# Kernel optimization log

Measured on AMD Instinct MI355X. Metric: run time of the kernel, lower is better.

Reference implementation:

```python
import jax, jax.numpy as jnp
import numpy as np


def _closest_dist_sum(p1, p2):
    # p1: [B, N, 3], p2: [B, M, 3]
    # Euclidean distance via the expanded quadratic form; matches
    # torch.norm(p1 - p2, 2, dim=3) -> min over p2 -> sum over all.
    d2 = (jnp.sum(p1 * p1, axis=-1)[:, :, None]
          + jnp.sum(p2 * p2, axis=-1)[:, None, :]
          - 2.0 * jnp.einsum('bnd,bmd->bnm', p1, p2))  # [B, N, M]
    d = jnp.sqrt(jnp.maximum(d2, 0.0))
    return jnp.sum(jnp.min(d, axis=2))


def setup_inputs() -> dict:
    key = jax.random.key(0)
    k1, k2 = jax.random.split(key)
    shape_xyz = jax.random.normal(k1, (8, 8192, 6), dtype=jnp.float32)
    skel_xyz = jax.random.normal(k2, (8, 2048, 3), dtype=jnp.float32)
    return {"shape_xyz": shape_xyz, "skel_xyz": skel_xyz}


def reference(shape_xyz, skel_xyz):
    # normals (shape_xyz[:, :, 3:6]) are extracted but unused in the loss
    pts = shape_xyz[:, :, :3]
    cd1 = _closest_dist_sum(pts, skel_xyz)   # shape -> skeleton
    cd2 = _closest_dist_sum(skel_xyz, pts)   # skeleton -> shape
    loss_cd = (cd1 + cd2) * 0.0001
    return loss_cd
```

## Files before the change

kernel.cpp:

```cpp
#include <hip/hip_runtime.h>

#define BATCH   8
#define SHAPE_N 8192
#define SKEL_M  2048
#define CHUNK   1024

#define WS2_OFF 512

typedef short bf16x8 __attribute__((ext_vector_type(8)));
typedef float f32x16 __attribute__((ext_vector_type(16)));
union FragU { bf16x8 v; uint4 u4; };

__device__ __forceinline__ unsigned int f2bf(float a) {
    unsigned int u = __float_as_uint(a);
    return (u + 0x7FFFu + ((u >> 16) & 1u)) >> 16;
}
__device__ __forceinline__ float bf2f(unsigned int h) {
    return __uint_as_float(h << 16);
}
__device__ __forceinline__ unsigned int pack2(unsigned int lo, unsigned int hi) {
    return lo | (hi << 16);
}
__device__ __forceinline__ void bfsplit(float v, unsigned int& h, unsigned int& l) {
    h = f2bf(v);
    l = f2bf(v - bf2f(h));
}

template <int SA, int SB>
__device__ __forceinline__ float cd_scan(
    const float* __restrict__ Araw,
    const float* __restrict__ Braw,
    uint4* sB, float* p_ra)
{
    const int tid = threadIdx.x;
    const int l = tid & 63;

    const float* p = Araw + (size_t)(l & 31) * SA;
    const float x = p[0], y = p[1], z = p[2];
    *p_ra = x * x + y * y + z * z;
    unsigned int hx, lx, hy, ly, hz, lz;
    bfsplit(x, hx, lx); bfsplit(y, hy, ly); bfsplit(z, hz, lz);
    const unsigned int one = 0x3F80u;
    FragU bf;
    if (l < 32) {
        bf.u4 = make_uint4(pack2(hx, hy), pack2(hz, one),
                           pack2(lx, ly), pack2(lz, one));
    } else {
        bf.u4 = make_uint4(pack2(hx, hy), pack2(hz, 0u), 0u, 0u);
    }

    const f32x16 Z = {0,0,0,0,0,0,0,0,0,0,0,0,0,0,0,0};
    float rmin = 3.4e38f;
    const unsigned int off0 = (unsigned int)((l >> 5) * 512 + (l & 31) * 16);

    for (int c = 0; c < 2048; c += CHUNK) {
        __syncthreads();
        const float* src = Braw + (size_t)c * SB;
        for (int i = tid; i < CHUNK; i += 256) {
            const float* q = src + (size_t)i * SB;
            const float bx = q[0], by = q[1], bz = q[2];
            const float cx = -2.f * bx, cy = -2.f * by, cz = -2.f * bz;
            const float rb = bx * bx + by * by + bz * bz;
            unsigned int chx, clx, chy, cly, chz, clz, rbh, rbl;
            bfsplit(cx, chx, clx); bfsplit(cy, chy, cly); bfsplit(cz, chz, clz);
            bfsplit(rb, rbh, rbl);
            const int g = i >> 5, r = i & 31;
            sB[g * 64 + r]      = make_uint4(pack2(chx, chy), pack2(chz, rbh),
                                             pack2(chx, chy), pack2(chz, rbl));
            sB[g * 64 + 32 + r] = make_uint4(pack2(clx, cly), pack2(clz, 0u),
                                             0u, 0u);
        }
        __syncthreads();

        unsigned int o = off0;
#pragma unroll 8
        for (int g = 0; g < CHUNK / 32; ++g) {
            FragU af;
            af.u4 = *(const uint4*)((const char*)sB + o);
            o += 1024;
            f32x16 D = __builtin_amdgcn_mfma_f32_32x32x16_bf16(af.v, bf.v, Z, 0, 0, 0);
            const float t0 = fminf(fminf(D[0],  D[1]),  D[2]);
            const float t1 = fminf(fminf(D[3],  D[4]),  D[5]);
            const float t2 = fminf(fminf(D[6],  D[7]),  D[8]);
            const float t3 = fminf(fminf(D[9],  D[10]), D[11]);
            const float t4 = fminf(fminf(D[12], D[13]), D[14]);
            const float u0 = fminf(fminf(t0, t1), t2);
            const float u1 = fminf(fminf(t3, t4), D[15]);
            rmin = fminf(rmin, fminf(u0, u1));
        }
    }
    rmin = fminf(rmin, __shfl_xor(rmin, 32, 64));
    return rmin;
}

__global__ __launch_bounds__(256) void cd_main(
    const float* __restrict__ shape, const float* __restrict__ skel,
    float* __restrict__ ws)
{
    __shared__ uint4 sB[CHUNK * 2];
    __shared__ float s_wsum[4];
    const int tid = threadIdx.x;
    const int l = tid & 63, wv = tid >> 6;
    const int bid = blockIdx.x;

    if (bid < 512) {
        const int b = bid >> 6, sub = bid & 63;
        float ra;
        const float rmin = cd_scan<6, 3>(
            shape + ((size_t)b * SHAPE_N + sub * 128 + wv * 32) * 6,
            skel + (size_t)b * SKEL_M * 3, sB, &ra);
        float d = (l < 32) ? sqrtf(fmaxf(ra + rmin, 0.f)) : 0.f;
        for (int o = 32; o; o >>= 1) d += __shfl_down(d, o, 64);
        if (l == 0) s_wsum[wv] = d;
        __syncthreads();
        if (tid == 0)
            ws[bid] = s_wsum[0] + s_wsum[1] + s_wsum[2] + s_wsum[3];
    } else {
        const int j = bid - 512;
        const int b = j >> 6, rem = j & 63;
        const int asub = rem >> 2, bs = rem & 3;
        float ra;
        const float rmin = cd_scan<3, 6>(
            skel + ((size_t)b * SKEL_M + asub * 128 + wv * 32) * 3,
            shape + ((size_t)b * SHAPE_N + bs * 2048) * 6, sB, &ra);
        if (l < 32)
            ws[WS2_OFF + bs * (BATCH * SKEL_M) + b * SKEL_M +
               asub * 128 + wv * 32 + l] = ra + rmin;
    }
}

__global__ __launch_bounds__(1024) void cd_reduce(
    const float* __restrict__ ws, float* __restrict__ out)
{
    __shared__ float s_wsum[16];
    const int t = threadIdx.x;
    float s = 0.f;

    const float4* w4 = (const float4*)(ws + WS2_OFF);
#pragma unroll
    for (int r = 0; r < 4; ++r) {
        const int i4 = r * 1024 + t;
        float4 v0 = w4[i4];
        const float4 v1 = w4[4096 + i4];
        const float4 v2 = w4[8192 + i4];
        const float4 v3 = w4[12288 + i4];
        v0.x = fminf(fminf(v0.x, v1.x), fminf(v2.x, v3.x));
        v0.y = fminf(fminf(v0.y, v1.y), fminf(v2.y, v3.y));
        v0.z = fminf(fminf(v0.z, v1.z), fminf(v2.z, v3.z));
        v0.w = fminf(fminf(v0.w, v1.w), fminf(v2.w, v3.w));
        s += sqrtf(fmaxf(v0.x, 0.f)) + sqrtf(fmaxf(v0.y, 0.f)) +
             sqrtf(fmaxf(v0.z, 0.f)) + sqrtf(fmaxf(v0.w, 0.f));
    }
    if (t < 512) s += ws[t];

    for (int o = 32; o; o >>= 1) s += __shfl_down(s, o, 64);
    const int lane = t & 63, wave = t >> 6;
    if (lane == 0) s_wsum[wave] = s;
    __syncthreads();
    if (t == 0) {
        float tot = 0.f;
#pragma unroll
        for (int w = 0; w < 16; ++w) tot += s_wsum[w];
        out[0] = tot * 1e-4f;
    }
}

extern "C" void kernel_launch(void* const* d_in, const int* in_sizes, int n_in,
                              void* d_out, int out_size, void* d_ws, size_t ws_size,
                              hipStream_t stream) {
    const float* shape = (const float*)d_in[0];
    const float* skel  = (const float*)d_in[1];
    float* out         = (float*)d_out;
    float* ws          = (float*)d_ws;

    cd_main<<<1024, 256, 0, stream>>>(shape, skel, ws);
    cd_reduce<<<1, 1024, 0, stream>>>(ws, out);
}
```

Before: 75.07 us.

## Precompute bf16 point fragments and double-buffer async LDS loads with register-blocked MFMA

A new prep kernel converts every skeleton and shape point into split-bf16 MFMA fragments once and writes them to workspace, so the main kernel no longer redoes this conversion in each block. The main kernel then streams those fragments into LDS with global_load_lds into a double buffer, overlapping the next chunk's load with the current chunk's compute. Each wave now holds four A fragments and splits the B range by wave, so one LDS read feeds four MFMAs; per-wave minima are merged through shared memory. The cost is an extra kernel launch, workspace traffic for the precomputed fragments, and more registers per wave.

Result: faster. 73.60 us (-2.0%).

```diff
diff --git a/kernel.cpp b/kernel.cpp
--- a/kernel.cpp
+++ b/kernel.cpp
@@ -3,9 +3,11 @@
 #define BATCH   8
 #define SHAPE_N 8192
 #define SKEL_M  2048
-#define CHUNK   1024
+#define CHUNK   512
 
 #define WS2_OFF 512
+#define SKC_OFF 66048
+#define SHC_OFF (66048 + 131072)
 
 typedef short bf16x8 __attribute__((ext_vector_type(8)));
 typedef float f32x16 __attribute__((ext_vector_type(16)));
@@ -26,106 +28,179 @@
     l = f2bf(v - bf2f(h));
 }
 
-template <int SA, int SB>
-__device__ __forceinline__ float cd_scan(
-    const float* __restrict__ Araw,
-    const float* __restrict__ Braw,
-    uint4* sB, float* p_ra)
-{
-    const int tid = threadIdx.x;
-    const int l = tid & 63;
-
-    const float* p = Araw + (size_t)(l & 31) * SA;
-    const float x = p[0], y = p[1], z = p[2];
-    *p_ra = x * x + y * y + z * z;
-    unsigned int hx, lx, hy, ly, hz, lz;
-    bfsplit(x, hx, lx); bfsplit(y, hy, ly); bfsplit(z, hz, lz);
-    const unsigned int one = 0x3F80u;
-    FragU bf;
-    if (l < 32) {
-        bf.u4 = make_uint4(pack2(hx, hy), pack2(hz, one),
-                           pack2(lx, ly), pack2(lz, one));
-    } else {
-        bf.u4 = make_uint4(pack2(hx, hy), pack2(hz, 0u), 0u, 0u);
-    }
-
-    const f32x16 Z = {0,0,0,0,0,0,0,0,0,0,0,0,0,0,0,0};
-    float rmin = 3.4e38f;
-    const unsigned int off0 = (unsigned int)((l >> 5) * 512 + (l & 31) * 16);
-
-    for (int c = 0; c < 2048; c += CHUNK) {
-        __syncthreads();
-        const float* src = Braw + (size_t)c * SB;
-        for (int i = tid; i < CHUNK; i += 256) {
-            const float* q = src + (size_t)i * SB;
-            const float bx = q[0], by = q[1], bz = q[2];
-            const float cx = -2.f * bx, cy = -2.f * by, cz = -2.f * bz;
-            const float rb = bx * bx + by * by + bz * bz;
-            unsigned int chx, clx, chy, cly, chz, clz, rbh, rbl;
-            bfsplit(cx, chx, clx); bfsplit(cy, chy, cly); bfsplit(cz, chz, clz);
-            bfsplit(rb, rbh, rbl);
-            const int g = i >> 5, r = i & 31;
-            sB[g * 64 + r]      = make_uint4(pack2(chx, chy), pack2(chz, rbh),
-                                             pack2(chx, chy), pack2(chz, rbl));
-            sB[g * 64 + 32 + r] = make_uint4(pack2(clx, cly), pack2(clz, 0u),
-                                             0u, 0u);
-        }
-        __syncthreads();
-
-        unsigned int o = off0;
-#pragma unroll 8
-        for (int g = 0; g < CHUNK / 32; ++g) {
-            FragU af;
-            af.u4 = *(const uint4*)((const char*)sB + o);
-            o += 1024;
-            f32x16 D = __builtin_amdgcn_mfma_f32_32x32x16_bf16(af.v, bf.v, Z, 0, 0, 0);
-            const float t0 = fminf(fminf(D[0],  D[1]),  D[2]);
-            const float t1 = fminf(fminf(D[3],  D[4]),  D[5]);
-            const float t2 = fminf(fminf(D[6],  D[7]),  D[8]);
-            const float t3 = fminf(fminf(D[9],  D[10]), D[11]);
-            const float t4 = fminf(fminf(D[12], D[13]), D[14]);
-            const float u0 = fminf(fminf(t0, t1), t2);
-            const float u1 = fminf(fminf(t3, t4), D[15]);
-            rmin = fminf(rmin, fminf(u0, u1));
-        }
-    }
-    rmin = fminf(rmin, __shfl_xor(rmin, 32, 64));
-    return rmin;
-}
-
-__global__ __launch_bounds__(256) void cd_main(
+__device__ __forceinline__ void conv_point(float bx, float by, float bz,
+                                           uint4& hi, uint4& lo) {
+    const float cx = -2.f * bx, cy = -2.f * by, cz = -2.f * bz;
+    const float rb = bx * bx + by * by + bz * bz;
+    unsigned int chx, clx, chy, cly, chz, clz, rbh, rbl;
+    bfsplit(cx, chx, clx); bfsplit(cy, chy, cly); bfsplit(cz, chz, clz);
+    bfsplit(rb, rbh, rbl);
+    hi = make_uint4(pack2(chx, chy), pack2(chz, rbh),
+                    pack2(chx, chy), pack2(chz, rbl));
+    lo = make_uint4(pack2(clx, cly), pack2(clz, 0u), 0u, 0u);
+}
+
+__device__ __forceinline__ void gl16(const char* g, char* l) {
+    __builtin_amdgcn_global_load_lds(
+        (const __attribute__((address_space(1))) void*)g,
+        (__attribute__((address_space(3))) void*)l, 16, 0, 0);
+}
+
+__global__ __launch_bounds__(256) void cd_prep(
     const float* __restrict__ shape, const float* __restrict__ skel,
     float* __restrict__ ws)
 {
-    __shared__ uint4 sB[CHUNK * 2];
-    __shared__ float s_wsum[4];
+    const int p = blockIdx.x * 256 + threadIdx.x;
+    const float* q;
+    uint4* dst;
+    int idx;
+    if (p < BATCH * SKEL_M) {
+        const int b = p >> 11; idx = p & (SKEL_M - 1);
+        q = skel + (size_t)p * 3;
+        dst = (uint4*)(ws + SKC_OFF) + (size_t)b * 4096;
+    } else {
+        const int s = p - BATCH * SKEL_M;
+        const int b = s >> 13; idx = s & (SHAPE_N - 1);
+        q = shape + (size_t)s * 6;
+        dst = (uint4*)(ws + SHC_OFF) + (size_t)b * 16384;
+    }
+    uint4 hi, lo;
+    conv_point(q[0], q[1], q[2], hi, lo);
+    const int g = idx >> 5, r = idx & 31;
+    dst[g * 64 + r]      = hi;
+    dst[g * 64 + 32 + r] = lo;
+}
+
+template <int SA>
+__device__ __forceinline__ void cd_scan2(
+    const float* __restrict__ Araw,
+    const uint4* __restrict__ Bconv,
+    uint4* __restrict__ sB,
+    float* rmin, float* ra)
+{
+    const int tid = threadIdx.x;
+    const int l = tid & 63, wv = tid >> 6;
+    const unsigned int one = 0x3F80u;
+
+    FragU bf[4];
+#pragma unroll
+    for (int j = 0; j < 4; ++j) {
+        const float* p = Araw + (size_t)(j * 32 + (l & 31)) * SA;
+        const float x = p[0], y = p[1], z = p[2];
+        ra[j] = x * x + y * y + z * z;
+        unsigned int hx, lx, hy, ly, hz, lz;
+        bfsplit(x, hx, lx); bfsplit(y, hy, ly); bfsplit(z, hz, lz);
+        if (l < 32)
+            bf[j].u4 = make_uint4(pack2(hx, hy), pack2(hz, one),
+                                  pack2(lx, ly), pack2(lz, one));
+        else
+            bf[j].u4 = make_uint4(pack2(hx, hy), pack2(hz, 0u), 0u, 0u);
+        rmin[j] = 3.4e38f;
+    }
+
+    const f32x16 Z = {0,0,0,0,0,0,0,0,0,0,0,0,0,0,0,0};
+    const char* gbase = (const char*)Bconv;
+    char* lbase = (char*)sB;
+
+#pragma unroll
+    for (int k = 0; k < 4; ++k)
+        gl16(gbase + k * 4096 + tid * 16, lbase + k * 4096 + tid * 16);
+    __syncthreads();
+
+    for (int c = 0; c < 4; ++c) {
+        if (c < 3) {
+            const char* src = gbase + (c + 1) * 16384;
+            char* dstl = lbase + (((c + 1) & 1) ? 16384 : 0);
+#pragma unroll
+            for (int k = 0; k < 4; ++k)
+                gl16(src + k * 4096 + tid * 16, dstl + k * 4096 + tid * 16);
+        }
+        unsigned int o = (unsigned int)(((c & 1) ? 16384 : 0) + wv * 4096 +
+                                        (l >> 5) * 512 + (l & 31) * 16);
+#pragma unroll
+        for (int g = 0; g < 4; ++g) {
+            FragU af;
+            af.u4 = *(const uint4*)(lbase + o);
+            o += 1024;
+#pragma unroll
+            for (int j = 0; j < 4; ++j) {
+                f32x16 D = __builtin_amdgcn_mfma_f32_32x32x16_bf16(
+                    af.v, bf[j].v, Z, 0, 0, 0);
+                const float t0 = fminf(fminf(D[0],  D[1]),  D[2]);
+                const float t1 = fminf(fminf(D[3],  D[4]),  D[5]);
+                const float t2 = fminf(fminf(D[6],  D[7]),  D[8]);
+                const float t3 = fminf(fminf(D[9],  D[10]), D[11]);
+                const float t4 = fminf(fminf(D[12], D[13]), D[14]);
+                const float u0 = fminf(fminf(t0, t1), t2);
+                const float u1 = fminf(fminf(t3, t4), D[15]);
+                rmin[j] = fminf(rmin[j], fminf(u0, u1));
+            }
+        }
+        __syncthreads();
+    }
+#pragma unroll
+    for (int j = 0; j < 4; ++j)
+        rmin[j] = fminf(rmin[j], __shfl_xor(rmin[j], 32, 64));
+}
+
+__global__ __launch_bounds__(256, 4) void cd_main(
+    const float* __restrict__ shape, const float* __restrict__ skel,
+    float* __restrict__ ws)
+{
+    __shared__ uint4 sB[CHUNK * 4];
+    __shared__ float smin[4][128];
+    __shared__ float sra[128];
+    __shared__ float s_wsum[2];
     const int tid = threadIdx.x;
     const int l = tid & 63, wv = tid >> 6;
     const int bid = blockIdx.x;
+    float rmin[4], ra[4];
 
     if (bid < 512) {
         const int b = bid >> 6, sub = bid & 63;
-        float ra;
-        const float rmin = cd_scan<6, 3>(
-            shape + ((size_t)b * SHAPE_N + sub * 128 + wv * 32) * 6,
-            skel + (size_t)b * SKEL_M * 3, sB, &ra);
-        float d = (l < 32) ? sqrtf(fmaxf(ra + rmin, 0.f)) : 0.f;
-        for (int o = 32; o; o >>= 1) d += __shfl_down(d, o, 64);
-        if (l == 0) s_wsum[wv] = d;
-        __syncthreads();
-        if (tid == 0)
-            ws[bid] = s_wsum[0] + s_wsum[1] + s_wsum[2] + s_wsum[3];
+        cd_scan2<6>(shape + ((size_t)b * SHAPE_N + sub * 128) * 6,
+                    (const uint4*)(ws + SKC_OFF) + (size_t)b * 4096,
+                    sB, rmin, ra);
     } else {
         const int j = bid - 512;
         const int b = j >> 6, rem = j & 63;
         const int asub = rem >> 2, bs = rem & 3;
-        float ra;
-        const float rmin = cd_scan<3, 6>(
-            skel + ((size_t)b * SKEL_M + asub * 128 + wv * 32) * 3,
-            shape + ((size_t)b * SHAPE_N + bs * 2048) * 6, sB, &ra);
-        if (l < 32)
+        cd_scan2<3>(skel + ((size_t)b * SKEL_M + asub * 128) * 3,
+                    (const uint4*)(ws + SHC_OFF) + (size_t)b * 16384 + bs * 4096,
+                    sB, rmin, ra);
+    }
+
+    if (l < 32) {
+#pragma unroll
+        for (int j = 0; j < 4; ++j) smin[wv][j * 32 + l] = rmin[j];
+        if (wv == 0) {
+#pragma unroll
+            for (int j = 0; j < 4; ++j) sra[j * 32 + l] = ra[j];
+        }
+    }
+    __syncthreads();
+
+    if (bid < 512) {
+        float d = 0.f;
+        if (tid < 128) {
+            const float m = fminf(fminf(smin[0][tid], smin[1][tid]),
+                                  fminf(smin[2][tid], smin[3][tid]));
+            d = sqrtf(fmaxf(sra[tid] + m, 0.f));
+        }
+        for (int o = 32; o; o >>= 1) d += __shfl_down(d, o, 64);
+        if (l == 0 && wv < 2) s_wsum[wv] = d;
+        __syncthreads();
+        if (tid == 0) ws[bid] = s_wsum[0] + s_wsum[1];
+    } else {
+        if (tid < 128) {
+            const int j = bid - 512;
+            const int b = j >> 6, rem = j & 63;
+            const int asub = rem >> 2, bs = rem & 3;
+            const float m = fminf(fminf(smin[0][tid], smin[1][tid]),
+                                  fminf(smin[2][tid], smin[3][tid]));
             ws[WS2_OFF + bs * (BATCH * SKEL_M) + b * SKEL_M +
-               asub * 128 + wv * 32 + l] = ra + rmin;
+               asub * 128 + tid] = sra[tid] + m;
+        }
     }
 }
 
@@ -173,6 +248,7 @@
     float* out         = (float*)d_out;
     float* ws          = (float*)d_ws;
 
+    cd_prep<<<320, 256, 0, stream>>>(shape, skel, ws);
     cd_main<<<1024, 256, 0, stream>>>(shape, skel, ws);
     cd_reduce<<<1, 1024, 0, stream>>>(ws, out);
 }
```
